# Kernel tuning notes

Hardware: AMD Instinct MI355X
Metric: run time of the kernel (lower is better)

Reference implementation:

```python
import jax, jax.numpy as jnp
import numpy as np

B, S, E, H, D = 4, 2048, 1024, 16, 64  # batch, seq (n_query==graph_size), embed, heads, qkv_dim


def setup_inputs() -> dict:
    key = jax.random.key(0)
    k1, k2, k3, k4, k5, k6 = jax.random.split(key, 6)
    q = jax.random.normal(k1, (B, S, E), dtype=jnp.float32)
    h = jax.random.normal(k2, (B, S, E), dtype=jnp.float32)
    # mask==True means attention NOT allowed (negative adjacency)
    mask = jax.random.randint(k3, (B, S, S), 0, 2) == 1
    scale = 0.02
    Wq = jax.random.normal(k4, (H * D, E), dtype=jnp.float32) * scale
    Wk = jax.random.normal(k5, (H * D, E), dtype=jnp.float32) * scale
    Wv = jax.random.normal(k6, (H * D, E), dtype=jnp.float32) * scale
    return {"q": q, "h": h, "mask": mask, "Wq": Wq, "Wk": Wk, "Wv": Wv}


def reference(q, h, mask, Wq, Wk, Wv):
    b, sq, e = q.shape
    sk = h.shape[1]
    hd = Wq.shape[0]
    heads = H
    d = hd // heads
    norm = 1.0 / jnp.sqrt(jnp.asarray(d, dtype=q.dtype))
    # Linear(bias=False): y = x @ W^T ; then reshape_by_heads -> (B, H, S, D)
    Q = (q @ Wq.T).reshape(b, sq, heads, d).transpose(0, 2, 1, 3)
    K = (h @ Wk.T).reshape(b, sk, heads, d).transpose(0, 2, 1, 3)
    V = (h @ Wv.T).reshape(b, sk, heads, d).transpose(0, 2, 1, 3)
    compat = norm * jnp.einsum("bhqd,bhkd->bhqk", Q, K)  # (B,H,Sq,Sk)
    compat = jnp.where(mask[:, None, :, :], -jnp.inf, compat)
    attn = jax.nn.softmax(compat, axis=-1)
    out_heads = jnp.einsum("bhqk,bhkd->bhqd", attn, V)
    # transpose(1,2) then concat heads -> (B, Sq, H*D)
    return out_heads.transpose(0, 2, 1, 3).reshape(b, sq, heads * d)
```

## Files before the change

kernel.cpp:

```cpp
#include <hip/hip_runtime.h>
#include <math.h>

#define Bb 4
#define Ss 2048
#define Ee 1024
#define Hh 16
#define Dd 64
#define HD (Hh * Dd)

typedef __attribute__((ext_vector_type(8))) _Float16 f16x8;
typedef __attribute__((ext_vector_type(4))) _Float16 f16x4;
typedef __attribute__((ext_vector_type(4))) float f32x4;

__device__ __forceinline__ void gl_lds16(const void* g, void* l) {
  __builtin_amdgcn_global_load_lds(
      (const __attribute__((address_space(1))) unsigned int*)g,
      (__attribute__((address_space(3))) unsigned int*)l, 16, 0, 0);
}

__global__ __launch_bounds__(256) void cvt_all(const float* __restrict__ q,
                                               const float* __restrict__ h,
                                               const float* __restrict__ wq,
                                               const float* __restrict__ wk,
                                               const float* __restrict__ wv,
                                               _Float16* __restrict__ qf,
                                               _Float16* __restrict__ hf,
                                               _Float16* __restrict__ wqf,
                                               _Float16* __restrict__ wkf,
                                               _Float16* __restrict__ wvf) {
  const int QH = (Bb * Ss * Ee) / 4;
  const int WM = (HD * Ee) / 4;
  int i = blockIdx.x * 256 + threadIdx.x;
  const float* src;
  _Float16* dst;
  int off;
  if (i < QH)                { src = q;  dst = qf;  off = i; }
  else if (i < 2 * QH)       { src = h;  dst = hf;  off = i - QH; }
  else if (i < 2 * QH + WM)  { src = wq; dst = wqf; off = i - 2 * QH; }
  else if (i < 2 * QH + 2 * WM) { src = wk; dst = wkf; off = i - 2 * QH - WM; }
  else                       { src = wv; dst = wvf; off = i - 2 * QH - 2 * WM; }
  float4 v = ((const float4*)src)[off];
  f16x4 o;
  o.x = (_Float16)v.x; o.y = (_Float16)v.y;
  o.z = (_Float16)v.z; o.w = (_Float16)v.w;
  *(f16x4*)(dst + 4 * (size_t)off) = o;
}

__global__ __launch_bounds__(256) void mask_pack(const int* __restrict__ mask,
                                                 unsigned long long* __restrict__ pm) {
  int g = blockIdx.x * 256 + threadIdx.x;
  unsigned long long bits = __ballot(mask[g] != 0);
  if ((threadIdx.x & 63) == 0) pm[g >> 6] = bits;
}

__global__ __launch_bounds__(512) void proj_qkv(const _Float16* __restrict__ qf,
                                                const _Float16* __restrict__ hf,
                                                const _Float16* __restrict__ Wqf,
                                                const _Float16* __restrict__ Wkf,
                                                const _Float16* __restrict__ Wvf,
                                                _Float16* __restrict__ Qb,
                                                _Float16* __restrict__ Kb,
                                                _Float16* __restrict__ Vb) {
  __shared__ _Float16 As[2][256 * 64];
  __shared__ _Float16 Bs[2][128 * 64];
  const int seg = blockIdx.z;
  const _Float16* A = (seg == 0) ? qf : hf;
  const _Float16* W = (seg == 0) ? Wqf : ((seg == 1) ? Wkf : Wvf);
  _Float16* Y       = (seg == 0) ? Qb  : ((seg == 1) ? Kb  : Vb);
  const float scale = (seg == 0) ? 0.18033688011112042f : 1.0f;

  const int tid = threadIdx.x;
  const int wv = tid >> 6, lane = tid & 63;
  const int quad = lane >> 4, l16 = lane & 15;
  const int wr = wv >> 1, wc = wv & 1;
  const int bm = blockIdx.y * 256, bn = blockIdx.x * 128;

  auto stage = [&](int buf, int k0) {
#pragma unroll
    for (int i = 0; i < 4; ++i) {
      int cb = wv * 64 + i * 512;
      int c = cb + lane;
      int row = c >> 3;
      int l = (c & 7) ^ (row & 7);
      gl_lds16(A + (size_t)(bm + row) * Ee + k0 + l * 8,
               (char*)&As[buf][0] + (size_t)cb * 16);
    }
#pragma unroll
    for (int i = 0; i < 2; ++i) {
      int cb = wv * 64 + i * 512;
      int c = cb + lane;
      int row = c >> 3;
      int l = (c & 7) ^ (row & 7);
      gl_lds16(W + (size_t)(bn + row) * Ee + k0 + l * 8,
               (char*)&Bs[buf][0] + (size_t)cb * 16);
    }
  };

  f32x4 acc[4][4];
#pragma unroll
  for (int i = 0; i < 4; ++i)
#pragma unroll
    for (int j = 0; j < 4; ++j) acc[i][j] = (f32x4){0.f, 0.f, 0.f, 0.f};

  stage(0, 0);
  const int NT = Ee / 64;
  for (int it = 0; it < NT; ++it) {
    const int buf = it & 1;
    if (it + 1 < NT) {
      stage(buf ^ 1, (it + 1) * 64);
      asm volatile("s_waitcnt vmcnt(6)\n\ts_barrier" ::: "memory");
    } else {
      asm volatile("s_waitcnt vmcnt(0)\n\ts_barrier" ::: "memory");
    }
#pragma unroll
    for (int s = 0; s < 2; ++s) {
      f16x8 af[4], bf[4];
#pragma unroll
      for (int i = 0; i < 4; ++i) {
        int row = wr * 64 + i * 16 + l16;
        int l = s * 4 + quad;
        af[i] = *(const f16x8*)&As[buf][row * 64 + ((l ^ (row & 7)) << 3)];
      }
#pragma unroll
      for (int j = 0; j < 4; ++j) {
        int row = wc * 64 + j * 16 + l16;
        int l = s * 4 + quad;
        bf[j] = *(const f16x8*)&Bs[buf][row * 64 + ((l ^ (row & 7)) << 3)];
      }
#pragma unroll
      for (int i = 0; i < 4; ++i)
#pragma unroll
        for (int j = 0; j < 4; ++j)
          acc[i][j] = __builtin_amdgcn_mfma_f32_16x16x32_f16(af[i], bf[j], acc[i][j], 0, 0, 0);
    }
    asm volatile("s_barrier" ::: "memory");
  }

#pragma unroll
  for (int i = 0; i < 4; ++i)
#pragma unroll
    for (int j = 0; j < 4; ++j)
#pragma unroll
      for (int reg = 0; reg < 4; ++reg) {
        int row = bm + wr * 64 + i * 16 + quad * 4 + reg;
        int col = bn + wc * 64 + j * 16 + l16;
        Y[(size_t)row * HD + col] = (_Float16)(acc[i][j][reg] * scale);
      }
}

__global__ __launch_bounds__(256) void vtrans(const unsigned short* __restrict__ Vb,
                                              unsigned short* __restrict__ Vt) {
  __shared__ unsigned short T[64][68];
  const int nx = blockIdx.x;
  const int my = blockIdx.y;
  const int m0 = my * 64, n0 = nx * 64;
  const int bsel = m0 >> 11, s0 = m0 & 2047;
  const int tid = threadIdx.x;
  const int r = tid >> 4, c4 = (tid & 15) << 2;
#pragma unroll
  for (int i = 0; i < 4; ++i) {
    ushort4 v = *(const ushort4*)(Vb + (size_t)(m0 + r + i * 16) * HD + n0 + c4);
    T[r + i * 16][c4 + 0] = v.x; T[r + i * 16][c4 + 1] = v.y;
    T[r + i * 16][c4 + 2] = v.z; T[r + i * 16][c4 + 3] = v.w;
  }
  __syncthreads();
#pragma unroll
  for (int i = 0; i < 4; ++i) {
    ushort4 o;
    o.x = T[c4 + 0][r + i * 16]; o.y = T[c4 + 1][r + i * 16];
    o.z = T[c4 + 2][r + i * 16]; o.w = T[c4 + 3][r + i * 16];
    *(ushort4*)(Vt + ((size_t)bsel * HD + n0 + r + i * 16) * Ss + s0 + c4) = o;
  }
}

__global__ __launch_bounds__(256) void attn_mfma2(const _Float16* __restrict__ Qb,
                                                  const _Float16* __restrict__ Kb,
                                                  const _Float16* __restrict__ Vt,
                                                  const unsigned long long* __restrict__ pm,
                                                  float* __restrict__ out) {
  const int bq = blockIdx.x;
  const int h  = blockIdx.y;
  const int b  = blockIdx.z;
  const int tid  = threadIdx.x;
  const int wv   = tid >> 6;
  const int lane = tid & 63;
  const int quad = lane >> 4;
  const int l16  = lane & 15;

  __shared__ _Float16 Ks[64][72];
  __shared__ _Float16 Vs[64][72];

  const int qglob = bq * 64 + wv * 16 + l16;
  const _Float16* qrow = Qb + ((size_t)b * Ss + qglob) * HD + h * Dd;
  const f16x8 qf0 = *(const f16x8*)(qrow + quad * 8);
  const f16x8 qf1 = *(const f16x8*)(qrow + 32 + quad * 8);

  const int r = tid >> 2, c = (tid & 3) << 4;
  const _Float16* kbase = Kb + ((size_t)b * Ss + r) * HD + h * Dd + c;
  const _Float16* vbase = Vt + (((size_t)b * Hh + h) * Dd + r) * Ss + c;

  const unsigned long long* pmrow = pm + ((size_t)b * Ss + qglob) * (Ss >> 6);

  f32x4 O[4] = {{0.f,0.f,0.f,0.f},{0.f,0.f,0.f,0.f},{0.f,0.f,0.f,0.f},{0.f,0.f,0.f,0.f}};
  float lsum = 0.f;

  f16x8 ka = *(const f16x8*)kbase;
  f16x8 kb2 = *(const f16x8*)(kbase + 8);
  f16x8 va = *(const f16x8*)vbase;
  f16x8 vb2 = *(const f16x8*)(vbase + 8);

  for (int kt = 0; kt < Ss; kt += 64) {
    __syncthreads();
    *(f16x8*)&Ks[r][c]     = ka;
    *(f16x8*)&Ks[r][c + 8] = kb2;
    *(f16x8*)&Vs[r][c]     = va;
    *(f16x8*)&Vs[r][c + 8] = vb2;
    {
      const int ktn = (kt + 64) & (Ss - 1);
      ka  = *(const f16x8*)(kbase + (size_t)ktn * HD);
      kb2 = *(const f16x8*)(kbase + (size_t)ktn * HD + 8);
      va  = *(const f16x8*)(vbase + ktn);
      vb2 = *(const f16x8*)(vbase + ktn + 8);
    }
    __syncthreads();

    f32x4 c4[4] = {{0.f,0.f,0.f,0.f},{0.f,0.f,0.f,0.f},{0.f,0.f,0.f,0.f},{0.f,0.f,0.f,0.f}};
#pragma unroll
    for (int sub = 0; sub < 4; ++sub) {
      f16x8 k0 = *(const f16x8*)&Ks[sub * 16 + l16][quad * 8];
      f16x8 k1 = *(const f16x8*)&Ks[sub * 16 + l16][32 + quad * 8];
      c4[sub] = __builtin_amdgcn_mfma_f32_16x16x32_f16(k0, qf0, c4[sub], 0, 0, 0);
      c4[sub] = __builtin_amdgcn_mfma_f32_16x16x32_f16(k1, qf1, c4[sub], 0, 0, 0);
    }

    const unsigned long long mq = pmrow[kt >> 6] >> (quad * 4);
    f16x4 pf[4];
#pragma unroll
    for (int sub = 0; sub < 4; ++sub)
#pragma unroll
      for (int reg = 0; reg < 4; ++reg) {
        float t = ((mq >> (sub * 16 + reg)) & 1ull) ? -3.0e38f : c4[sub][reg];
        float p = __builtin_amdgcn_exp2f(t);
        lsum += p;
        pf[sub][reg] = (_Float16)p;
      }

#pragma unroll
    for (int dt = 0; dt < 4; ++dt)
#pragma unroll
      for (int sub = 0; sub < 4; ++sub) {
        f16x4 vf = *(const f16x4*)&Vs[dt * 16 + l16][sub * 16 + quad * 4];
        O[dt] = __builtin_amdgcn_mfma_f32_16x16x16f16(vf, pf[sub], O[dt], 0, 0, 0);
      }
  }

  lsum += __shfl_xor(lsum, 16, 64);
  lsum += __shfl_xor(lsum, 32, 64);
  const float inv = 1.0f / lsum;

  float* obase = out + ((size_t)b * Ss + qglob) * HD + h * Dd;
#pragma unroll
  for (int dt = 0; dt < 4; ++dt) {
    float4 st;
    st.x = O[dt][0] * inv; st.y = O[dt][1] * inv;
    st.z = O[dt][2] * inv; st.w = O[dt][3] * inv;
    *(float4*)(obase + dt * 16 + quad * 4) = st;
  }
}

extern "C" void kernel_launch(void* const* d_in, const int* in_sizes, int n_in,
                              void* d_out, int out_size, void* d_ws, size_t ws_size,
                              hipStream_t stream) {
  const float* q    = (const float*)d_in[0];
  const float* h    = (const float*)d_in[1];
  const int*   mask = (const int*)d_in[2];
  const float* Wq   = (const float*)d_in[3];
  const float* Wk   = (const float*)d_in[4];
  const float* Wv   = (const float*)d_in[5];
  float* out = (float*)d_out;

  char* ws = (char*)d_ws;
  const size_t MB = 1024 * 1024;
  _Float16* qf  = (_Float16*)(ws);
  _Float16* hf  = (_Float16*)(ws + 16 * MB);
  _Float16* Wqf = (_Float16*)(ws + 32 * MB);
  _Float16* Wkf = (_Float16*)(ws + 34 * MB);
  _Float16* Wvf = (_Float16*)(ws + 36 * MB);
  _Float16* Qb  = (_Float16*)(ws + 38 * MB);
  _Float16* Kb  = (_Float16*)(ws + 54 * MB);
  _Float16* Vb  = (_Float16*)(ws + 70 * MB);
  _Float16* Vt  = (_Float16*)(ws);
  unsigned long long* pm = (unsigned long long*)(ws + 86 * MB);

  const int total4 = 2 * (Bb * Ss * Ee) / 4 + 3 * (HD * Ee) / 4;
  cvt_all<<<total4 / 256, 256, 0, stream>>>(q, h, Wq, Wk, Wv, qf, hf, Wqf, Wkf, Wvf);

  mask_pack<<<(Bb * Ss * Ss) / 256, 256, 0, stream>>>(mask, pm);

  proj_qkv<<<dim3(HD / 128, (Bb * Ss) / 256, 3), 512, 0, stream>>>(
      qf, hf, Wqf, Wkf, Wvf, Qb, Kb, Vb);

  vtrans<<<dim3(HD / 64, (Bb * Ss) / 64), 256, 0, stream>>>((const unsigned short*)Vb,
                                                            (unsigned short*)Vt);

  attn_mfma2<<<dim3(Ss / 64, Hh, Bb), 256, 0, stream>>>(Qb, Kb, Vt, pm, out);
}
```

Baseline: 398.2 us.

## Fuse prep kernels, remap projection blocks per XCD, double query rows per attention wave

Merges the fp16 conversion and mask bit-packing kernels into one launch, with each mask wave now packing four 64-bit words. The projection GEMM grid is flattened and remapped so consecutive block IDs (likely dispatched round-robin across the 8 XCDs) cover row stripes, which may improve L2 reuse of A/W tiles. The attention kernel now gives each wave 32 query rows instead of 16, halving the number of blocks and the K/V LDS staging per query. Probabilities are packed with cvt_pkrtz. Doubling the accumulators raises register pressure and may lower occupancy.

```diff
diff --git a/kernel.cpp b/kernel.cpp
--- a/kernel.cpp
+++ b/kernel.cpp
@@ -10,6 +10,7 @@
 
 typedef __attribute__((ext_vector_type(8))) _Float16 f16x8;
 typedef __attribute__((ext_vector_type(4))) _Float16 f16x4;
+typedef __attribute__((ext_vector_type(2))) _Float16 f16x2;
 typedef __attribute__((ext_vector_type(4))) float f32x4;
 
 __device__ __forceinline__ void gl_lds16(const void* g, void* l) {
@@ -18,39 +19,50 @@
       (__attribute__((address_space(3))) unsigned int*)l, 16, 0, 0);
 }
 
-__global__ __launch_bounds__(256) void cvt_all(const float* __restrict__ q,
-                                               const float* __restrict__ h,
-                                               const float* __restrict__ wq,
-                                               const float* __restrict__ wk,
-                                               const float* __restrict__ wv,
-                                               _Float16* __restrict__ qf,
-                                               _Float16* __restrict__ hf,
-                                               _Float16* __restrict__ wqf,
-                                               _Float16* __restrict__ wkf,
-                                               _Float16* __restrict__ wvf) {
-  const int QH = (Bb * Ss * Ee) / 4;
-  const int WM = (HD * Ee) / 4;
-  int i = blockIdx.x * 256 + threadIdx.x;
-  const float* src;
-  _Float16* dst;
-  int off;
-  if (i < QH)                { src = q;  dst = qf;  off = i; }
-  else if (i < 2 * QH)       { src = h;  dst = hf;  off = i - QH; }
-  else if (i < 2 * QH + WM)  { src = wq; dst = wqf; off = i - 2 * QH; }
-  else if (i < 2 * QH + 2 * WM) { src = wk; dst = wkf; off = i - 2 * QH - WM; }
-  else                       { src = wv; dst = wvf; off = i - 2 * QH - 2 * WM; }
-  float4 v = ((const float4*)src)[off];
-  f16x4 o;
-  o.x = (_Float16)v.x; o.y = (_Float16)v.y;
-  o.z = (_Float16)v.z; o.w = (_Float16)v.w;
-  *(f16x4*)(dst + 4 * (size_t)off) = o;
-}
-
-__global__ __launch_bounds__(256) void mask_pack(const int* __restrict__ mask,
-                                                 unsigned long long* __restrict__ pm) {
-  int g = blockIdx.x * 256 + threadIdx.x;
-  unsigned long long bits = __ballot(mask[g] != 0);
-  if ((threadIdx.x & 63) == 0) pm[g >> 6] = bits;
+__device__ __forceinline__ f16x2 pkrtz(float a, float b) {
+  return __builtin_bit_cast(f16x2, __builtin_amdgcn_cvt_pkrtz(a, b));
+}
+
+#define CVT_BLOCKS 19456
+__global__ __launch_bounds__(256) void prep_all(const float* __restrict__ q,
+                                                const float* __restrict__ h,
+                                                const float* __restrict__ wq,
+                                                const float* __restrict__ wk,
+                                                const float* __restrict__ wv,
+                                                _Float16* __restrict__ qf,
+                                                _Float16* __restrict__ hf,
+                                                _Float16* __restrict__ wqf,
+                                                _Float16* __restrict__ wkf,
+                                                _Float16* __restrict__ wvf,
+                                                const int* __restrict__ mask,
+                                                unsigned long long* __restrict__ pm) {
+  if (blockIdx.x < CVT_BLOCKS) {
+    const int QH = (Bb * Ss * Ee) / 4;
+    const int WM = (HD * Ee) / 4;
+    int i = blockIdx.x * 256 + threadIdx.x;
+    const float* src;
+    _Float16* dst;
+    int off;
+    if (i < QH)                   { src = q;  dst = qf;  off = i; }
+    else if (i < 2 * QH)          { src = h;  dst = hf;  off = i - QH; }
+    else if (i < 2 * QH + WM)     { src = wq; dst = wqf; off = i - 2 * QH; }
+    else if (i < 2 * QH + 2 * WM) { src = wk; dst = wkf; off = i - 2 * QH - WM; }
+    else                          { src = wv; dst = wvf; off = i - 2 * QH - 2 * WM; }
+    float4 v = ((const float4*)src)[off];
+    f16x4 o;
+    o.x = (_Float16)v.x; o.y = (_Float16)v.y;
+    o.z = (_Float16)v.z; o.w = (_Float16)v.w;
+    *(f16x4*)(dst + 4 * (size_t)off) = o;
+  } else {
+    const int bid = blockIdx.x - CVT_BLOCKS;
+    const int wv = threadIdx.x >> 6, lane = threadIdx.x & 63;
+    const size_t base = ((size_t)bid * 4 + wv) * 256;
+#pragma unroll
+    for (int i = 0; i < 4; ++i) {
+      unsigned long long bits = __ballot(mask[base + i * 64 + lane] != 0);
+      if (lane == 0) pm[(base >> 6) + i] = bits;
+    }
+  }
 }
 
 __global__ __launch_bounds__(512) void proj_qkv(const _Float16* __restrict__ qf,
@@ -63,17 +75,22 @@
                                                 _Float16* __restrict__ Vb) {
   __shared__ _Float16 As[2][256 * 64];
   __shared__ _Float16 Bs[2][128 * 64];
-  const int seg = blockIdx.z;
+  const int seg = blockIdx.y;
   const _Float16* A = (seg == 0) ? qf : hf;
   const _Float16* W = (seg == 0) ? Wqf : ((seg == 1) ? Wkf : Wvf);
   _Float16* Y       = (seg == 0) ? Qb  : ((seg == 1) ? Kb  : Vb);
   const float scale = (seg == 0) ? 0.18033688011112042f : 1.0f;
 
+  const int lid = blockIdx.x;
+  const int xcd = lid & 7, m = lid >> 3;
+  const int stripe = xcd + 8 * (m & 3);
+  const int nt = m >> 2;
+  const int bm = stripe * 256, bn = nt * 128;
+
   const int tid = threadIdx.x;
   const int wv = tid >> 6, lane = tid & 63;
   const int quad = lane >> 4, l16 = lane & 15;
   const int wr = wv >> 1, wc = wv & 1;
-  const int bm = blockIdx.y * 256, bn = blockIdx.x * 128;
 
   auto stage = [&](int buf, int k0) {
 #pragma unroll
@@ -173,7 +190,7 @@
   }
 }
 
-__global__ __launch_bounds__(256) void attn_mfma2(const _Float16* __restrict__ Qb,
+__global__ __launch_bounds__(256) void attn_mfma3(const _Float16* __restrict__ Qb,
                                                   const _Float16* __restrict__ Kb,
                                                   const _Float16* __restrict__ Vt,
                                                   const unsigned long long* __restrict__ pm,
@@ -190,19 +207,28 @@
   __shared__ _Float16 Ks[64][72];
   __shared__ _Float16 Vs[64][72];
 
-  const int qglob = bq * 64 + wv * 16 + l16;
-  const _Float16* qrow = Qb + ((size_t)b * Ss + qglob) * HD + h * Dd;
-  const f16x8 qf0 = *(const f16x8*)(qrow + quad * 8);
-  const f16x8 qf1 = *(const f16x8*)(qrow + 32 + quad * 8);
+  const int q0g = bq * 128 + wv * 32;
+  f16x8 qf[2][2];
+#pragma unroll
+  for (int g = 0; g < 2; ++g) {
+    const _Float16* qrow = Qb + ((size_t)b * Ss + q0g + g * 16 + l16) * HD + h * Dd;
+    qf[g][0] = *(const f16x8*)(qrow + quad * 8);
+    qf[g][1] = *(const f16x8*)(qrow + 32 + quad * 8);
+  }
 
   const int r = tid >> 2, c = (tid & 3) << 4;
   const _Float16* kbase = Kb + ((size_t)b * Ss + r) * HD + h * Dd + c;
   const _Float16* vbase = Vt + (((size_t)b * Hh + h) * Dd + r) * Ss + c;
 
-  const unsigned long long* pmrow = pm + ((size_t)b * Ss + qglob) * (Ss >> 6);
-
-  f32x4 O[4] = {{0.f,0.f,0.f,0.f},{0.f,0.f,0.f,0.f},{0.f,0.f,0.f,0.f},{0.f,0.f,0.f,0.f}};
-  float lsum = 0.f;
+  const unsigned long long* pmrow0 = pm + ((size_t)b * Ss + q0g + l16) * (Ss >> 6);
+  const size_t pmg = (size_t)16 * (Ss >> 6);
+
+  f32x4 O[2][4];
+#pragma unroll
+  for (int g = 0; g < 2; ++g)
+#pragma unroll
+    for (int dt = 0; dt < 4; ++dt) O[g][dt] = (f32x4){0.f, 0.f, 0.f, 0.f};
+  float lsum[2] = {0.f, 0.f};
 
   f16x8 ka = *(const f16x8*)kbase;
   f16x8 kb2 = *(const f16x8*)(kbase + 8);
@@ -224,47 +250,66 @@
     }
     __syncthreads();
 
-    f32x4 c4[4] = {{0.f,0.f,0.f,0.f},{0.f,0.f,0.f,0.f},{0.f,0.f,0.f,0.f},{0.f,0.f,0.f,0.f}};
+    f32x4 c4[2][4];
+#pragma unroll
+    for (int g = 0; g < 2; ++g)
+#pragma unroll
+      for (int sub = 0; sub < 4; ++sub) c4[g][sub] = (f32x4){0.f, 0.f, 0.f, 0.f};
 #pragma unroll
     for (int sub = 0; sub < 4; ++sub) {
       f16x8 k0 = *(const f16x8*)&Ks[sub * 16 + l16][quad * 8];
       f16x8 k1 = *(const f16x8*)&Ks[sub * 16 + l16][32 + quad * 8];
-      c4[sub] = __builtin_amdgcn_mfma_f32_16x16x32_f16(k0, qf0, c4[sub], 0, 0, 0);
-      c4[sub] = __builtin_amdgcn_mfma_f32_16x16x32_f16(k1, qf1, c4[sub], 0, 0, 0);
-    }
-
-    const unsigned long long mq = pmrow[kt >> 6] >> (quad * 4);
-    f16x4 pf[4];
-#pragma unroll
-    for (int sub = 0; sub < 4; ++sub)
-#pragma unroll
-      for (int reg = 0; reg < 4; ++reg) {
-        float t = ((mq >> (sub * 16 + reg)) & 1ull) ? -3.0e38f : c4[sub][reg];
-        float p = __builtin_amdgcn_exp2f(t);
-        lsum += p;
-        pf[sub][reg] = (_Float16)p;
-      }
+#pragma unroll
+      for (int g = 0; g < 2; ++g) {
+        c4[g][sub] = __builtin_amdgcn_mfma_f32_16x16x32_f16(k0, qf[g][0], c4[g][sub], 0, 0, 0);
+        c4[g][sub] = __builtin_amdgcn_mfma_f32_16x16x32_f16(k1, qf[g][1], c4[g][sub], 0, 0, 0);
+      }
+    }
+
+    f16x4 pf[2][4];
+#pragma unroll
+    for (int g = 0; g < 2; ++g) {
+      const unsigned long long mq = pmrow0[(g ? pmg : 0) + (kt >> 6)] >> (quad * 4);
+#pragma unroll
+      for (int sub = 0; sub < 4; ++sub) {
+        float p[4];
+#pragma unroll
+        for (int reg = 0; reg < 4; ++reg) {
+          float t = ((mq >> (sub * 16 + reg)) & 1ull) ? -3.0e38f : c4[g][sub][reg];
+          p[reg] = __builtin_amdgcn_exp2f(t);
+          lsum[g] += p[reg];
+        }
+        f16x2 lo = pkrtz(p[0], p[1]);
+        f16x2 hi = pkrtz(p[2], p[3]);
+        pf[g][sub] = __builtin_shufflevector(lo, hi, 0, 1, 2, 3);
+      }
+    }
 
 #pragma unroll
     for (int dt = 0; dt < 4; ++dt)
 #pragma unroll
       for (int sub = 0; sub < 4; ++sub) {
         f16x4 vf = *(const f16x4*)&Vs[dt * 16 + l16][sub * 16 + quad * 4];
-        O[dt] = __builtin_amdgcn_mfma_f32_16x16x16f16(vf, pf[sub], O[dt], 0, 0, 0);
-      }
-  }
-
-  lsum += __shfl_xor(lsum, 16, 64);
-  lsum += __shfl_xor(lsum, 32, 64);
-  const float inv = 1.0f / lsum;
-
-  float* obase = out + ((size_t)b * Ss + qglob) * HD + h * Dd;
-#pragma unroll
-  for (int dt = 0; dt < 4; ++dt) {
-    float4 st;
-    st.x = O[dt][0] * inv; st.y = O[dt][1] * inv;
-    st.z = O[dt][2] * inv; st.w = O[dt][3] * inv;
-    *(float4*)(obase + dt * 16 + quad * 4) = st;
+#pragma unroll
+        for (int g = 0; g < 2; ++g)
+          O[g][dt] = __builtin_amdgcn_mfma_f32_16x16x16f16(vf, pf[g][sub], O[g][dt], 0, 0, 0);
+      }
+  }
+
+#pragma unroll
+  for (int g = 0; g < 2; ++g) {
+    float ls = lsum[g];
+    ls += __shfl_xor(ls, 16, 64);
+    ls += __shfl_xor(ls, 32, 64);
+    const float inv = 1.0f / ls;
+    float* obase = out + ((size_t)b * Ss + q0g + g * 16 + l16) * HD + h * Dd;
+#pragma unroll
+    for (int dt = 0; dt < 4; ++dt) {
+      float4 st;
+      st.x = O[g][dt][0] * inv; st.y = O[g][dt][1] * inv;
+      st.z = O[g][dt][2] * inv; st.w = O[g][dt][3] * inv;
+      *(float4*)(obase + dt * 16 + quad * 4) = st;
+    }
   }
 }
 
@@ -292,16 +337,14 @@
   _Float16* Vt  = (_Float16*)(ws);
   unsigned long long* pm = (unsigned long long*)(ws + 86 * MB);
 
-  const int total4 = 2 * (Bb * Ss * Ee) / 4 + 3 * (HD * Ee) / 4;
-  cvt_all<<<total4 / 256, 256, 0, stream>>>(q, h, Wq, Wk, Wv, qf, hf, Wqf, Wkf, Wvf);
-
-  mask_pack<<<(Bb * Ss * Ss) / 256, 256, 0, stream>>>(mask, pm);
-
-  proj_qkv<<<dim3(HD / 128, (Bb * Ss) / 256, 3), 512, 0, stream>>>(
-      qf, hf, Wqf, Wkf, Wvf, Qb, Kb, Vb);
+  const int mask_blocks = (Bb * Ss * Ss) / 1024;
+  prep_all<<<CVT_BLOCKS + mask_blocks, 256, 0, stream>>>(
+      q, h, Wq, Wk, Wv, qf, hf, Wqf, Wkf, Wvf, mask, pm);
+
+  proj_qkv<<<dim3(256, 3), 512, 0, stream>>>(qf, hf, Wqf, Wkf, Wvf, Qb, Kb, Vb);
 
   vtrans<<<dim3(HD / 64, (Bb * Ss) / 64), 256, 0, stream>>>((const unsigned short*)Vb,
                                                             (unsigned short*)Vt);
 
-  attn_mfma2<<<dim3(Ss / 64, Hh, Bb), 256, 0, stream>>>(Qb, Kb, Vt, pm, out);
-}
+  attn_mfma3<<<dim3(Ss / 128, Hh, Bb), 256, 0, stream>>>(Qb, Kb, Vt, pm, out);
+}
```

Result: faster. 367.8 us (-7.6%).
